# Kernel tuning notes

Hardware: AMD Instinct MI355X
Metric: run time of the kernel (lower is better)

The kernel has to match this reference:

```python
import jax, jax.numpy as jnp
import numpy as np

NEG_INF = -9e15
LEAKY_SLOPE = 0.01  # torch F.leaky_relu default


def setup_inputs() -> dict:
    key = jax.random.key(0)
    k1, k2, k3, k4 = jax.random.split(key, 4)
    N, F = 8192, 128
    inp = jax.random.normal(k1, (N, F), dtype=jnp.float32)
    adj = jax.random.randint(k2, (N, N), 0, 2, dtype=jnp.int32)
    # xavier_uniform with gain=1.414
    gain = 1.414
    limW = gain * np.sqrt(6.0 / (F + F))
    W = jax.random.uniform(k3, (F, F), minval=-limW, maxval=limW, dtype=jnp.float32)
    lima = gain * np.sqrt(6.0 / (2 * F + 1))
    a = jax.random.uniform(k4, (2 * F, 1), minval=-lima, maxval=lima, dtype=jnp.float32)
    return {"input": inp, "adj": adj, "W": W, "a": a}


def reference(input, adj, W, a):
    F_ = W.shape[0]
    h = input @ W                               # [N, F]
    # a_input[i,j] = concat(h[i], h[j]); (a_input @ a)[i,j] = h[i]@a1 + h[j]@a2
    a1, a2 = a[:F_, 0], a[F_:, 0]               # [F], [F]
    s1 = h @ a1                                 # [N]
    s2 = h @ a2                                 # [N]
    e = jax.nn.leaky_relu(s1[:, None] + s2[None, :], negative_slope=LEAKY_SLOPE)  # [N, N]
    masked = jnp.where(adj > 0, e, jnp.float32(NEG_INF))
    attention = jax.nn.softmax(masked, axis=1)  # [N, N]
    return attention @ h                        # [N, F]
```

## Files before the change

### kernel.cpp

```cpp
#include <hip/hip_runtime.h>
#include <hip/hip_bf16.h>

#define NN 8192
#define FF 128

typedef unsigned short ushort_t;
typedef __attribute__((ext_vector_type(4))) float f32x4;
typedef __attribute__((ext_vector_type(4))) int i32x4;
typedef __attribute__((ext_vector_type(8))) short s16x8;

__global__ __launch_bounds__(256)
void k1_hw(const float* __restrict__ inp, const float* __restrict__ W,
           const float* __restrict__ a, ushort_t* __restrict__ hT,
           float* __restrict__ s1g, float* __restrict__ Ug, float* __restrict__ Vg)
{
  __shared__ float Wl[FF * FF];
  __shared__ float il[32 * 129];
  __shared__ float red1[32 * 8];
  __shared__ float red2[32 * 8];
  const int t = threadIdx.x;
  const int ib = blockIdx.x * 32;

  {
    const float4* Ws = (const float4*)W;
    float4* Wd = (float4*)Wl;
#pragma unroll
    for (int q = 0; q < 16; ++q) Wd[t + 256 * q] = Ws[t + 256 * q];
  }
#pragma unroll
  for (int q = 0; q < 4; ++q) {
    int idx = t + 256 * q;
    int r = idx >> 5, c4 = idx & 31;
    float4 v = ((const float4*)(inp + (size_t)(ib + r) * FF))[c4];
    float* dst = &il[r * 129 + c4 * 4];
    dst[0] = v.x; dst[1] = v.y; dst[2] = v.z; dst[3] = v.w;
  }
  __syncthreads();

  const int r = t & 31;
  const int c0 = (t >> 5) * 16;
  float acc[16];
#pragma unroll
  for (int j = 0; j < 16; ++j) acc[j] = 0.f;

#pragma unroll 4
  for (int k = 0; k < FF; ++k) {
    float iv = il[r * 129 + k];
    const float4* wrow = (const float4*)&Wl[k * FF + c0];
    float4 w0 = wrow[0], w1 = wrow[1], w2 = wrow[2], w3 = wrow[3];
    acc[0]  += iv * w0.x; acc[1]  += iv * w0.y; acc[2]  += iv * w0.z; acc[3]  += iv * w0.w;
    acc[4]  += iv * w1.x; acc[5]  += iv * w1.y; acc[6]  += iv * w1.z; acc[7]  += iv * w1.w;
    acc[8]  += iv * w2.x; acc[9]  += iv * w2.y; acc[10] += iv * w2.z; acc[11] += iv * w2.w;
    acc[12] += iv * w3.x; acc[13] += iv * w3.y; acc[14] += iv * w3.z; acc[15] += iv * w3.w;
  }

  float ps1 = 0.f, ps2 = 0.f;
#pragma unroll
  for (int q = 0; q < 4; ++q) {
    float4 a1v = *(const float4*)(a + c0 + 4 * q);
    float4 a2v = *(const float4*)(a + FF + c0 + 4 * q);
    ps1 += acc[4*q+0]*a1v.x + acc[4*q+1]*a1v.y + acc[4*q+2]*a1v.z + acc[4*q+3]*a1v.w;
    ps2 += acc[4*q+0]*a2v.x + acc[4*q+1]*a2v.y + acc[4*q+2]*a2v.z + acc[4*q+3]*a2v.w;
  }
  red1[r * 8 + (t >> 5)] = ps1;
  red2[r * 8 + (t >> 5)] = ps2;

#pragma unroll
  for (int j = 0; j < 16; ++j) {
    unsigned b = __float_as_uint(acc[j]);
    hT[(unsigned)(c0 + j) * NN + (unsigned)(ib + r)] = (ushort_t)((b + 0x8000u) >> 16);
  }
  __syncthreads();
  if (t < 32) {
    float s1 = 0.f, s2 = 0.f;
#pragma unroll
    for (int g2 = 0; g2 < 8; ++g2) { s1 += red1[t * 8 + g2]; s2 += red2[t * 8 + g2]; }
    s1g[ib + t] = s1;
    Ug[ib + t] = expf(s2);
    Vg[ib + t] = expf(0.01f * s2);
  }
}

__global__ __launch_bounds__(512, 4)
void k3_attn(const int* __restrict__ adj, const float* __restrict__ s1g,
             const float* __restrict__ Ug, const float* __restrict__ Vg,
             const ushort_t* __restrict__ hT, float* __restrict__ out)
{
  __shared__ __align__(16) char smem[65536];
  __shared__ float zL[8][16];

  const int t = threadIdx.x;
  const int lane = t & 63, w = t >> 6;
  const int rowl = lane & 15, kq = lane >> 4;
  const int rb = blockIdx.x * 16;
  const int jb0 = w * 1024;

  const float s1v = s1g[rb + rowl];
  const float lv = s1v > 0.f ? s1v : 0.01f * s1v;
  const float P = expf(s1v - lv - 24.f);
  const float Q = expf(0.01f * s1v - lv - 24.f);
  const float E = expf(-s1v);

  f32x4 acc[8], acc9;
#pragma unroll
  for (int n = 0; n < 8; ++n) { acc[n][0] = 0.f; acc[n][1] = 0.f; acc[n][2] = 0.f; acc[n][3] = 0.f; }
  acc9[0] = 0.f; acc9[1] = 0.f; acc9[2] = 0.f; acc9[3] = 0.f;

  char* wt = smem + w * 8192;

  const ushort_t* hp[8];
#pragma unroll
  for (int n = 0; n < 8; ++n) hp[n] = hT + (size_t)(n * 16 + rowl) * NN + jb0 + kq * 8;

  union { unsigned u[4]; s16x8 v; } onesu;
  onesu.u[0] = 0x3F803F80u; onesu.u[1] = 0x3F803F80u;
  onesu.u[2] = 0x3F803F80u; onesu.u[3] = 0x3F803F80u;
  const s16x8 ones = onesu.v;

  const int wr_off = (((lane >> 1)) << 4) + ((lane & 1) << 3);
  const int aoff = rowl * 512;

  for (int sub = 0; sub < 4; ++sub) {
    const int jbase = jb0 + sub * 256;
    const float4 Uq = *(const float4*)(Ug + jbase + lane * 4);
    const float4 Vq = *(const float4*)(Vg + jbase + lane * 4);

#pragma unroll
    for (int r = 0; r < 16; ++r) {
      const i32x4 A = *((const i32x4*)(adj + (size_t)(rb + r) * NN + jbase) + lane);
      const float Pr = __shfl(P, r);
      const float Qr = __shfl(Q, r);
      const float Er = __shfl(E, r);
      float w0 = Uq.x > Er ? Pr * Uq.x : Qr * Vq.x;  w0 = A[0] > 0 ? w0 : 0.f;
      float w1 = Uq.y > Er ? Pr * Uq.y : Qr * Vq.y;  w1 = A[1] > 0 ? w1 : 0.f;
      float w2 = Uq.z > Er ? Pr * Uq.z : Qr * Vq.z;  w2 = A[2] > 0 ? w2 : 0.f;
      float w3 = Uq.w > Er ? Pr * Uq.w : Qr * Vq.w;  w3 = A[3] > 0 ? w3 : 0.f;
      unsigned p0 = ((__float_as_uint(w0) + 0x8000u) >> 16) | ((__float_as_uint(w1) + 0x8000u) & 0xFFFF0000u);
      unsigned p1 = ((__float_as_uint(w2) + 0x8000u) >> 16) | ((__float_as_uint(w3) + 0x8000u) & 0xFFFF0000u);
      *(uint2*)(wt + r * 512 + (wr_off ^ ((r & 7) << 4))) = make_uint2(p0, p1);
    }

#pragma unroll
    for (int kc = 0; kc < 8; ++kc) {
      const s16x8 af = *(const s16x8*)(wt + aoff + (((kc * 4 + kq) ^ (rowl & 7)) << 4));
#pragma unroll
      for (int n = 0; n < 8; ++n) {
        const s16x8 bf = *(const s16x8*)(hp[n] + sub * 256 + kc * 32);
        acc[n] = __builtin_amdgcn_mfma_f32_16x16x32_bf16(af, bf, acc[n], 0, 0, 0);
      }
      acc9 = __builtin_amdgcn_mfma_f32_16x16x32_bf16(af, ones, acc9, 0, 0, 0);
    }
  }

  if (rowl == 0) {
#pragma unroll
    for (int r2 = 0; r2 < 4; ++r2) zL[w][kq * 4 + r2] = acc9[r2];
  }
  float* accW = (float*)(smem + w * 8192);
#pragma unroll
  for (int n = 0; n < 8; ++n)
#pragma unroll
    for (int r2 = 0; r2 < 4; ++r2)
      accW[(kq * 4 + r2) * 128 + n * 16 + rowl] = acc[n][r2];
  __syncthreads();

  {
    const int idx = t * 4;
    const int row = idx >> 7, col = idx & 127;
    f32x4 s; s[0] = 0.f; s[1] = 0.f; s[2] = 0.f; s[3] = 0.f;
    float zs = 0.f;
#pragma unroll
    for (int w2 = 0; w2 < 8; ++w2) {
      s += *(const f32x4*)(smem + w2 * 8192 + ((row * 128 + col) << 2));
      zs += zL[w2][row];
    }
    const float rz = 1.f / zs;
    float4 o;
    o.x = s[0] * rz; o.y = s[1] * rz; o.z = s[2] * rz; o.w = s[3] * rz;
    *(float4*)(out + (size_t)(rb + row) * FF + col) = o;
  }
}

extern "C" void kernel_launch(void* const* d_in, const int* in_sizes, int n_in,
                              void* d_out, int out_size, void* d_ws, size_t ws_size,
                              hipStream_t stream)
{
  const float* inp = (const float*)d_in[0];
  const int* adj   = (const int*)d_in[1];
  const float* W   = (const float*)d_in[2];
  const float* a   = (const float*)d_in[3];
  float* out = (float*)d_out;

  char* ws = (char*)d_ws;
  ushort_t* hT = (ushort_t*)ws;
  float* s1g = (float*)(ws + (size_t)(2u << 20));
  float* Ug  = (float*)(ws + (size_t)(2u << 20) + (32u << 10));
  float* Vg  = (float*)(ws + (size_t)(2u << 20) + (64u << 10));

  hipLaunchKernelGGL(k1_hw, dim3(256), dim3(256), 0, stream, inp, W, a, hT, s1g, Ug, Vg);
  hipLaunchKernelGGL(k3_attn, dim3(512), dim3(512), 0, stream, adj, s1g, Ug, Vg, hT, out);
}
```

Before: 519.8 us.

## Pack adjacency into bitmasks and restructure attention kernel with double-buffered weight tiles

Adds a pre-pass kernel that packs the int32 adjacency matrix into 64-bit ballot bitmasks. The attention kernel then reads the compact masks instead of the full int matrix. The attention kernel is also reorganized: each wave now owns a 16-column slice of the output over all keys rather than a key slice, which removes the cross-wave reduction. Weight tiles are built in LDS with double buffering, overlapping the next window's loads with the MFMAs, and h is stored in a blocked layout. The pack pass still reads adj once in full, so the int traffic remains; the gain has to come from the restructured attention kernel.

New measurement: 525.1 us. About the same (+1.0%).

```diff
diff --git a/kernel.cpp b/kernel.cpp
--- a/kernel.cpp
+++ b/kernel.cpp
@@ -8,10 +8,33 @@
 typedef __attribute__((ext_vector_type(4))) float f32x4;
 typedef __attribute__((ext_vector_type(4))) int i32x4;
 typedef __attribute__((ext_vector_type(8))) short s16x8;
+typedef __attribute__((ext_vector_type(2))) unsigned long long u64x2;
+
+__device__ __forceinline__ void block_sync_lds() {
+  asm volatile("s_waitcnt lgkmcnt(0)\n\ts_barrier" ::: "memory");
+}
+
+__global__ __launch_bounds__(256)
+void k0_pack(const int* __restrict__ adj, unsigned long long* __restrict__ bits)
+{
+  const int lane = threadIdx.x & 63;
+  const int wid = (blockIdx.x * 256 + threadIdx.x) >> 6;
+  for (int blk = wid; blk < (NN / 256) * NN; blk += 8192) {
+    const i32x4 a = *((const i32x4*)adj + (size_t)blk * 64 + lane);
+    unsigned long long m0 = __ballot(a[0] > 0);
+    unsigned long long m1 = __ballot(a[1] > 0);
+    unsigned long long m2 = __ballot(a[2] > 0);
+    unsigned long long m3 = __ballot(a[3] > 0);
+    if (lane < 4) {
+      unsigned long long v = lane == 0 ? m0 : lane == 1 ? m1 : lane == 2 ? m2 : m3;
+      bits[(size_t)blk * 4 + lane] = v;
+    }
+  }
+}
 
 __global__ __launch_bounds__(256)
 void k1_hw(const float* __restrict__ inp, const float* __restrict__ W,
-           const float* __restrict__ a, ushort_t* __restrict__ hT,
+           const float* __restrict__ a, ushort_t* __restrict__ hB,
            float* __restrict__ s1g, float* __restrict__ Ug, float* __restrict__ Vg)
 {
   __shared__ float Wl[FF * FF];
@@ -68,7 +91,8 @@
 #pragma unroll
   for (int j = 0; j < 16; ++j) {
     unsigned b = __float_as_uint(acc[j]);
-    hT[(unsigned)(c0 + j) * NN + (unsigned)(ib + r)] = (ushort_t)((b + 0x8000u) >> 16);
+    hB[((size_t)blockIdx.x * 128 + (c0 + j)) * 32 + ((r >> 3) & 3) * 8 + (r & 7)] =
+        (ushort_t)((b + 0x8000u) >> 16);
   }
   __syncthreads();
   if (t < 32) {
@@ -82,102 +106,109 @@
 }
 
 __global__ __launch_bounds__(512, 4)
-void k3_attn(const int* __restrict__ adj, const float* __restrict__ s1g,
+void k3_attn(const unsigned long long* __restrict__ bits, const float* __restrict__ s1g,
              const float* __restrict__ Ug, const float* __restrict__ Vg,
-             const ushort_t* __restrict__ hT, float* __restrict__ out)
-{
-  __shared__ __align__(16) char smem[65536];
-  __shared__ float zL[8][16];
+             const ushort_t* __restrict__ hB, float* __restrict__ out)
+{
+  __shared__ ushort_t wtile[2][16][1024];
+  __shared__ float zL[16];
 
   const int t = threadIdx.x;
   const int lane = t & 63, w = t >> 6;
   const int rowl = lane & 15, kq = lane >> 4;
   const int rb = blockIdx.x * 16;
-  const int jb0 = w * 1024;
-
-  const float s1v = s1g[rb + rowl];
-  const float lv = s1v > 0.f ? s1v : 0.01f * s1v;
-  const float P = expf(s1v - lv - 24.f);
-  const float Q = expf(0.01f * s1v - lv - 24.f);
-  const float E = expf(-s1v);
-
-  f32x4 acc[8], acc9;
-#pragma unroll
-  for (int n = 0; n < 8; ++n) { acc[n][0] = 0.f; acc[n][1] = 0.f; acc[n][2] = 0.f; acc[n][3] = 0.f; }
+  const int r0 = 2 * w, r1 = 2 * w + 1;
+
+  const float s1a = s1g[rb + r0];
+  const float s1b = s1g[rb + r1];
+  const float la = s1a > 0.f ? s1a : 0.01f * s1a;
+  const float lb = s1b > 0.f ? s1b : 0.01f * s1b;
+  const float Pa = expf(s1a - la - 24.f), Qa = expf(0.01f * s1a - la - 24.f), Ea = expf(-s1a);
+  const float Pb = expf(s1b - lb - 24.f), Qb = expf(0.01f * s1b - lb - 24.f), Eb = expf(-s1b);
+
+  f32x4 acc, acc9;
+  acc[0] = 0.f; acc[1] = 0.f; acc[2] = 0.f; acc[3] = 0.f;
   acc9[0] = 0.f; acc9[1] = 0.f; acc9[2] = 0.f; acc9[3] = 0.f;
-
-  char* wt = smem + w * 8192;
-
-  const ushort_t* hp[8];
-#pragma unroll
-  for (int n = 0; n < 8; ++n) hp[n] = hT + (size_t)(n * 16 + rowl) * NN + jb0 + kq * 8;
 
   union { unsigned u[4]; s16x8 v; } onesu;
   onesu.u[0] = 0x3F803F80u; onesu.u[1] = 0x3F803F80u;
   onesu.u[2] = 0x3F803F80u; onesu.u[3] = 0x3F803F80u;
   const s16x8 ones = onesu.v;
 
-  const int wr_off = (((lane >> 1)) << 4) + ((lane & 1) << 3);
-  const int aoff = rowl * 512;
-
-  for (int sub = 0; sub < 4; ++sub) {
-    const int jbase = jb0 + sub * 256;
-    const float4 Uq = *(const float4*)(Ug + jbase + lane * 4);
-    const float4 Vq = *(const float4*)(Vg + jbase + lane * 4);
-
-#pragma unroll
-    for (int r = 0; r < 16; ++r) {
-      const i32x4 A = *((const i32x4*)(adj + (size_t)(rb + r) * NN + jbase) + lane);
-      const float Pr = __shfl(P, r);
-      const float Qr = __shfl(Q, r);
-      const float Er = __shfl(E, r);
-      float w0 = Uq.x > Er ? Pr * Uq.x : Qr * Vq.x;  w0 = A[0] > 0 ? w0 : 0.f;
-      float w1 = Uq.y > Er ? Pr * Uq.y : Qr * Vq.y;  w1 = A[1] > 0 ? w1 : 0.f;
-      float w2 = Uq.z > Er ? Pr * Uq.z : Qr * Vq.z;  w2 = A[2] > 0 ? w2 : 0.f;
-      float w3 = Uq.w > Er ? Pr * Uq.w : Qr * Vq.w;  w3 = A[3] > 0 ? w3 : 0.f;
-      unsigned p0 = ((__float_as_uint(w0) + 0x8000u) >> 16) | ((__float_as_uint(w1) + 0x8000u) & 0xFFFF0000u);
-      unsigned p1 = ((__float_as_uint(w2) + 0x8000u) >> 16) | ((__float_as_uint(w3) + 0x8000u) & 0xFFFF0000u);
-      *(uint2*)(wt + r * 512 + (wr_off ^ ((r & 7) << 4))) = make_uint2(p0, p1);
-    }
-
-#pragma unroll
-    for (int kc = 0; kc < 8; ++kc) {
-      const s16x8 af = *(const s16x8*)(wt + aoff + (((kc * 4 + kq) ^ (rowl & 7)) << 4));
-#pragma unroll
-      for (int n = 0; n < 8; ++n) {
-        const s16x8 bf = *(const s16x8*)(hp[n] + sub * 256 + kc * 32);
-        acc[n] = __builtin_amdgcn_mfma_f32_16x16x32_bf16(af, bf, acc[n], 0, 0, 0);
+  float4 Uq[4], Vq[4];
+  u64x2 Ga[4], Gb[4], Gc[4], Gd[4];
+
+  auto stage_load = [&](int win) {
+    const int jw = win * 1024;
+    const unsigned long long* bp0 = bits + (size_t)(rb + r0) * 128 + (jw >> 6);
+    const unsigned long long* bp1 = bits + (size_t)(rb + r1) * 128 + (jw >> 6);
+#pragma unroll
+    for (int q = 0; q < 4; ++q) {
+      Uq[q] = *(const float4*)(Ug + jw + q * 256 + lane * 4);
+      Vq[q] = *(const float4*)(Vg + jw + q * 256 + lane * 4);
+      Ga[q] = *(const u64x2*)(bp0 + q * 4);
+      Gb[q] = *(const u64x2*)(bp0 + q * 4 + 2);
+      Gc[q] = *(const u64x2*)(bp1 + q * 4);
+      Gd[q] = *(const u64x2*)(bp1 + q * 4 + 2);
+    }
+  };
+
+  auto stage_write = [&](int tb) {
+    char* base0 = (char*)wtile + tb * 32768 + r0 * 2048;
+    char* base1 = (char*)wtile + tb * 32768 + r1 * 2048;
+    const int sw0 = (r0 & 7) << 4, sw1 = (r1 & 7) << 4;
+#pragma unroll
+    for (int q = 0; q < 4; ++q) {
+      {
+        float w0 = ((Ga[q][0] >> lane) & 1) ? (Uq[q].x > Ea ? Pa * Uq[q].x : Qa * Vq[q].x) : 0.f;
+        float w1 = ((Ga[q][1] >> lane) & 1) ? (Uq[q].y > Ea ? Pa * Uq[q].y : Qa * Vq[q].y) : 0.f;
+        float w2 = ((Gb[q][0] >> lane) & 1) ? (Uq[q].z > Ea ? Pa * Uq[q].z : Qa * Vq[q].z) : 0.f;
+        float w3 = ((Gb[q][1] >> lane) & 1) ? (Uq[q].w > Ea ? Pa * Uq[q].w : Qa * Vq[q].w) : 0.f;
+        unsigned p0 = ((__float_as_uint(w0) + 0x8000u) >> 16) | ((__float_as_uint(w1) + 0x8000u) & 0xFFFF0000u);
+        unsigned p1 = ((__float_as_uint(w2) + 0x8000u) >> 16) | ((__float_as_uint(w3) + 0x8000u) & 0xFFFF0000u);
+        *(uint2*)(base0 + ((q * 512 + lane * 8) ^ sw0)) = make_uint2(p0, p1);
       }
+      {
+        float w0 = ((Gc[q][0] >> lane) & 1) ? (Uq[q].x > Eb ? Pb * Uq[q].x : Qb * Vq[q].x) : 0.f;
+        float w1 = ((Gc[q][1] >> lane) & 1) ? (Uq[q].y > Eb ? Pb * Uq[q].y : Qb * Vq[q].y) : 0.f;
+        float w2 = ((Gd[q][0] >> lane) & 1) ? (Uq[q].z > Eb ? Pb * Uq[q].z : Qb * Vq[q].z) : 0.f;
+        float w3 = ((Gd[q][1] >> lane) & 1) ? (Uq[q].w > Eb ? Pb * Uq[q].w : Qb * Vq[q].w) : 0.f;
+        unsigned p0 = ((__float_as_uint(w0) + 0x8000u) >> 16) | ((__float_as_uint(w1) + 0x8000u) & 0xFFFF0000u);
+        unsigned p1 = ((__float_as_uint(w2) + 0x8000u) >> 16) | ((__float_as_uint(w3) + 0x8000u) & 0xFFFF0000u);
+        *(uint2*)(base1 + ((q * 512 + lane * 8) ^ sw1)) = make_uint2(p0, p1);
+      }
+    }
+  };
+
+  stage_load(0);
+  stage_write(0);
+  block_sync_lds();
+
+  for (int win = 0; win < 8; ++win) {
+    if (win < 7) stage_load(win + 1);
+    const char* wbuf = (const char*)wtile + (win & 1) * 32768;
+    const ushort_t* hp = hB + (size_t)(win * 32) * 4096 + (w * 16 + rowl) * 32 + kq * 8;
+#pragma unroll 8
+    for (int kc = 0; kc < 32; ++kc) {
+      const s16x8 af = *(const s16x8*)(wbuf + rowl * 2048 + (((kc * 4 + kq) ^ (rowl & 7)) << 4));
+      const s16x8 bf = *(const s16x8*)(hp + (size_t)kc * 4096);
+      acc  = __builtin_amdgcn_mfma_f32_16x16x32_bf16(af, bf,   acc,  0, 0, 0);
       acc9 = __builtin_amdgcn_mfma_f32_16x16x32_bf16(af, ones, acc9, 0, 0, 0);
     }
-  }
-
-  if (rowl == 0) {
-#pragma unroll
-    for (int r2 = 0; r2 < 4; ++r2) zL[w][kq * 4 + r2] = acc9[r2];
-  }
-  float* accW = (float*)(smem + w * 8192);
-#pragma unroll
-  for (int n = 0; n < 8; ++n)
-#pragma unroll
-    for (int r2 = 0; r2 < 4; ++r2)
-      accW[(kq * 4 + r2) * 128 + n * 16 + rowl] = acc[n][r2];
+    if (win < 7) stage_write((win + 1) & 1);
+    block_sync_lds();
+  }
+
+  if (w == 0 && rowl == 0) {
+#pragma unroll
+    for (int r2 = 0; r2 < 4; ++r2) zL[kq * 4 + r2] = acc9[r2];
+  }
   __syncthreads();
 
-  {
-    const int idx = t * 4;
-    const int row = idx >> 7, col = idx & 127;
-    f32x4 s; s[0] = 0.f; s[1] = 0.f; s[2] = 0.f; s[3] = 0.f;
-    float zs = 0.f;
-#pragma unroll
-    for (int w2 = 0; w2 < 8; ++w2) {
-      s += *(const f32x4*)(smem + w2 * 8192 + ((row * 128 + col) << 2));
-      zs += zL[w2][row];
-    }
-    const float rz = 1.f / zs;
-    float4 o;
-    o.x = s[0] * rz; o.y = s[1] * rz; o.z = s[2] * rz; o.w = s[3] * rz;
-    *(float4*)(out + (size_t)(rb + row) * FF + col) = o;
+#pragma unroll
+  for (int r2 = 0; r2 < 4; ++r2) {
+    const int row = kq * 4 + r2;
+    out[(size_t)(rb + row) * FF + w * 16 + rowl] = acc[r2] * (1.f / zL[row]);
   }
 }
 
@@ -192,11 +223,13 @@
   float* out = (float*)d_out;
 
   char* ws = (char*)d_ws;
-  ushort_t* hT = (ushort_t*)ws;
+  ushort_t* hB = (ushort_t*)ws;
   float* s1g = (float*)(ws + (size_t)(2u << 20));
   float* Ug  = (float*)(ws + (size_t)(2u << 20) + (32u << 10));
   float* Vg  = (float*)(ws + (size_t)(2u << 20) + (64u << 10));
-
-  hipLaunchKernelGGL(k1_hw, dim3(256), dim3(256), 0, stream, inp, W, a, hT, s1g, Ug, Vg);
-  hipLaunchKernelGGL(k3_attn, dim3(512), dim3(512), 0, stream, adj, s1g, Ug, Vg, hT, out);
-}
+  unsigned long long* bits = (unsigned long long*)(ws + (size_t)(3u << 20));
+
+  hipLaunchKernelGGL(k0_pack, dim3(2048), dim3(256), 0, stream, adj, bits);
+  hipLaunchKernelGGL(k1_hw, dim3(256), dim3(256), 0, stream, inp, W, a, hB, s1g, Ug, Vg);
+  hipLaunchKernelGGL(k3_attn, dim3(512), dim3(512), 0, stream, bits, s1g, Ug, Vg, hB, out);
+}
```
